# Kernel optimization log

Measured on AMD Instinct MI355X. Metric: run time of the kernel, lower is better.

The kernel has to match this reference:

```python
import jax, jax.numpy as jnp
import numpy as np
from jax import lax

N_HEADS = 16
EPS = 1e-6
CHUNK = 128  # chunk size for the causal kv cumsum scan


def causal_dot_product(q, k, v):
    """Equivalent to cumsum over outer-products: out[l] = q[l] . sum_{j<=l} k[j] v[j]^T.
    Chunked lax.scan avoids materializing the [B,H,L,D,M] tensor.
    q,k: [B,H,L,D], v: [B,H,L,M] -> [B,H,L,M]."""
    B, H, L, D = q.shape
    M = v.shape[-1]
    nc = L // CHUNK
    qc = q.reshape(B, H, nc, CHUNK, D).transpose(2, 0, 1, 3, 4)
    kc = k.reshape(B, H, nc, CHUNK, D).transpose(2, 0, 1, 3, 4)
    vc = v.reshape(B, H, nc, CHUNK, M).transpose(2, 0, 1, 3, 4)

    def step(kv_carry, inp):
        qb, kb, vb = inp  # [B,H,C,D], [B,H,C,D], [B,H,C,M]
        kv = jnp.einsum('bhcd,bhcm->bhcdm', kb, vb)
        kv_cum = jnp.cumsum(kv, axis=2) + kv_carry[:, :, None]
        out = jnp.einsum('bhcd,bhcdm->bhcm', qb, kv_cum)
        return kv_cum[:, :, -1], out

    init = jnp.zeros((B, H, D, M), q.dtype)
    _, outs = lax.scan(step, init, (qc, kc, vc))  # outs: [nc,B,H,C,M]
    return outs.transpose(1, 2, 0, 3, 4).reshape(B, H, L, M)


def flow_attention_causal(x, Wq, bq, Wk, bk, Wv, bv, Wo, bo):
    B, L, _ = x.shape
    d_model = Wq.shape[1]
    H = N_HEADS
    # projections -> [B,H,L,D]
    q = (x @ Wq + bq).reshape(B, L, H, -1).transpose(0, 2, 1, 3)
    k = (x @ Wk + bk).reshape(B, L, H, -1).transpose(0, 2, 1, 3)
    v = (x @ Wv + bv).reshape(B, L, H, -1).transpose(0, 2, 1, 3)
    # kernel_method = sigmoid
    q = jax.nn.sigmoid(q)
    k = jax.nn.sigmoid(k)

    sink_incoming = 1.0 / jnp.einsum('bhld,bhld->bhl', q + EPS, jnp.cumsum(k, axis=2) + EPS)
    source_outgoing = 1.0 / jnp.einsum('bhld,bhld->bhl', k + EPS, jnp.cumsum(q, axis=2) + EPS)
    normal = (jnp.arange(L, dtype=x.dtype) + 1.0)[None, None, :]  # [1,1,L]
    sink_incoming = sink_incoming * normal
    source_outgoing = source_outgoing * normal

    conserved_sink = jnp.einsum(
        'bhld,bhld->bhl', q + EPS,
        jnp.cumsum(k * source_outgoing[..., None], axis=2) + EPS) / normal
    conserved_source = jnp.einsum(
        'bhld,bhld->bhl', k + EPS,
        jnp.cumsum(q * sink_incoming[..., None], axis=2) + EPS) / normal

    sink_allocation = jax.nn.sigmoid(conserved_sink)
    cs = jnp.exp(conserved_source)
    source_competition = cs / jnp.cumsum(cs, axis=-1) * normal

    out = causal_dot_product(
        q * (sink_incoming / normal)[..., None],
        k,
        v * source_competition[..., None]) * sink_allocation[..., None]
    out = out.transpose(0, 2, 1, 3).reshape(B, L, d_model)
    return out @ Wo + bo  # dropout is identity at eval


def setup_inputs() -> dict:
    key = jax.random.key(0)
    ks = jax.random.split(key, 9)
    B, L, d_model = 4, 4096, 1024
    s = 0.02
    return {
        'x': jax.random.normal(ks[0], (B, L, d_model), dtype=jnp.float32),
        'Wq': jax.random.normal(ks[1], (d_model, d_model), dtype=jnp.float32) * s,
        'bq': jnp.zeros((d_model,), dtype=jnp.float32),
        'Wk': jax.random.normal(ks[2], (d_model, d_model), dtype=jnp.float32) * s,
        'bk': jnp.zeros((d_model,), dtype=jnp.float32),
        'Wv': jax.random.normal(ks[3], (d_model, d_model), dtype=jnp.float32) * s,
        'bv': jnp.zeros((d_model,), dtype=jnp.float32),
        'Wo': jax.random.normal(ks[4], (d_model, d_model), dtype=jnp.float32) * s,
        'bo': jnp.zeros((d_model,), dtype=jnp.float32),
    }


def reference(x, Wq, bq, Wk, bk, Wv, bv, Wo, bo):
    return flow_attention_causal(x, Wq, bq, Wk, bk, Wv, bv, Wo, bo)
```

## Files before the change

kernel.cpp:

```cpp
#include <hip/hip_runtime.h>
#include <stdint.h>

#define B_ 4
#define L_ 4096
#define DM 1024
#define H_ 16
#define D_ 64
#define BH (B_*H_)
#define N_ (B_*L_)
#define CS 128
#define NC (L_/CS)
#define SC 64
#define NSC (L_/SC)
#define EPSF 1e-6f

typedef unsigned short u16;
typedef unsigned int   u32;
typedef __attribute__((ext_vector_type(8))) short s16x8;
typedef __attribute__((ext_vector_type(4))) float f32x4;

__device__ __forceinline__ float bf2f(u16 u){
  union { u32 i; float f; } v; v.i = ((u32)u) << 16; return v.f;
}
__device__ __forceinline__ u16 f2bf(float f){
  union { float f; u32 i; } v; v.f = f;
  u32 i = v.i;
  return (u16)((i + 0x7fffu + ((i >> 16) & 1u)) >> 16);
}
__device__ __forceinline__ void gload16(const void* g, void* l){
  __builtin_amdgcn_global_load_lds(
      (const __attribute__((address_space(1))) u32*)g,
      (__attribute__((address_space(3))) u32*)l, 16, 0, 0);
}
__device__ __forceinline__ f32x4 mfma16(s16x8 a, s16x8 b, f32x4 c){
  return __builtin_amdgcn_mfma_f32_16x16x32_bf16(a, b, c, 0, 0, 0);
}
__device__ __forceinline__ float sigmoidf_(float x){ return 1.0f/(1.0f+__expf(-x)); }

__global__ void cvt_kernel(const float* __restrict__ in, u16* __restrict__ out, int n4){
  int i = blockIdx.x * blockDim.x + threadIdx.x;
  if (i >= n4) return;
  float4 v = ((const float4*)in)[i];
  union { u16 s[4]; uint2 u; } o;
  o.s[0]=f2bf(v.x); o.s[1]=f2bf(v.y); o.s[2]=f2bf(v.z); o.s[3]=f2bf(v.w);
  ((uint2*)out)[i] = o.u;
}

__global__ __launch_bounds__(256) void transpose_w4_kernel(
    const float* __restrict__ Wq, const float* __restrict__ Wk,
    const float* __restrict__ Wv, const float* __restrict__ Wo,
    u16* __restrict__ wqkvT, u16* __restrict__ woT){
  __shared__ float t[64][65];
  int z = blockIdx.z;
  const float* W = (z==0) ? Wq : (z==1) ? Wk : (z==2) ? Wv : Wo;
  u16* WT = (z<3) ? (wqkvT + (size_t)z*DM*DM) : woT;
  int n0 = blockIdx.x * 64, k0 = blockIdx.y * 64;
  int tx = threadIdx.x & 63, ty = threadIdx.x >> 6;
  #pragma unroll
  for (int s = 0; s < 64; s += 4)
    t[ty + s][tx] = W[(size_t)(k0 + ty + s) * DM + n0 + tx];
  __syncthreads();
  #pragma unroll
  for (int s = 0; s < 64; s += 4)
    WT[(size_t)(n0 + ty + s) * DM + k0 + tx] = f2bf(t[tx][ty + s]);
}

template<int QKV>
__global__ __launch_bounds__(512, 2) void gemm256_kernel(
    const u16* __restrict__ A, const u16* __restrict__ BT,
    const float* __restrict__ biasq, const float* __restrict__ biask, const float* __restrict__ biasv,
    u16* __restrict__ oq, u16* __restrict__ ok, u16* __restrict__ ov,
    float* __restrict__ outf,
    float* __restrict__ sumQ, float* __restrict__ sumK, int NBY)
{
  __shared__ __align__(16) u16 smem[65536];
  char* smb = (char*)smem;
  int tid = threadIdx.x;
  int wave = tid >> 6, lane = tid & 63;
  int wm = wave >> 2, wn = wave & 3;
  int nwg = gridDim.x;
  int q8 = nwg >> 3;
  int id = blockIdx.x;
  int id2 = (id & 7) * q8 + (id >> 3);
  int bx = id2 / NBY, by = id2 % NBY;
  int m0 = bx * 256, n0 = by * 256;
  int srcq = (tid & 7) ^ ((tid >> 3) & 7);
  const u16* aRow = A  + (size_t)(m0 + (tid >> 3)) * 1024 + srcq * 8;
  const u16* bRow = BT + (size_t)(n0 + (tid >> 3)) * 1024 + srcq * 8;

  f32x4 acc[8][4];
  #pragma unroll
  for (int i=0;i<8;i++)
    #pragma unroll
    for (int j=0;j<4;j++) acc[i][j] = (f32x4){0.f,0.f,0.f,0.f};

  int fr = lane & 15, q = lane >> 4;
  int aoff0 = fr*128 + (((q ^ (lane&3)) + 4*((lane>>2)&1)) << 4);
  int aoff1 = fr*128 + (((q ^ (lane&3)) + 4*(1 ^ ((lane>>2)&1))) << 4);

  #define STAGE(s, t) { \
    _Pragma("unroll") \
    for (int i_ = 0; i_ < 4; i_++){ \
      gload16(aRow + (size_t)(t)*64 + (size_t)i_*65536, smb + (s)*32768 + i_*8192 + tid*16); \
      gload16(bRow + (size_t)(t)*64 + (size_t)i_*65536, smb + 65536 + (s)*32768 + i_*8192 + tid*16); \
    } }

  #define COMPUTE(s) { \
    const char* Ab_ = smb + (s)*32768 + wm*16384; \
    const char* Bb_ = smb + 65536 + (s)*32768 + wn*8192; \
    _Pragma("unroll") \
    for (int kk_ = 0; kk_ < 2; kk_++){ \
      int off_ = kk_ ? aoff1 : aoff0; \
      s16x8 af_[8], bf_[4]; \
      _Pragma("unroll") \
      for (int mi_ = 0; mi_ < 8; mi_++) af_[mi_] = *(const s16x8*)(Ab_ + mi_*2048 + off_); \
      _Pragma("unroll") \
      for (int ni_ = 0; ni_ < 4; ni_++) bf_[ni_] = *(const s16x8*)(Bb_ + ni_*2048 + off_); \
      _Pragma("unroll") \
      for (int mi_ = 0; mi_ < 8; mi_++) \
        _Pragma("unroll") \
        for (int ni_ = 0; ni_ < 4; ni_++) \
          acc[mi_][ni_] = mfma16(af_[mi_], bf_[ni_], acc[mi_][ni_]); \
    } }

  STAGE(0, 0)
  STAGE(1, 1)
  for (int t = 0; t < 14; t++){
    asm volatile("s_waitcnt vmcnt(8)" ::: "memory");
    __builtin_amdgcn_s_barrier();
    asm volatile("" ::: "memory");
    COMPUTE(t & 1)
    asm volatile("s_waitcnt lgkmcnt(0)" ::: "memory");
    __builtin_amdgcn_s_barrier();
    asm volatile("" ::: "memory");
    STAGE(t & 1, t + 2)
  }
  asm volatile("s_waitcnt vmcnt(8)" ::: "memory");
  __builtin_amdgcn_s_barrier();
  asm volatile("" ::: "memory");
  COMPUTE(0)
  asm volatile("s_waitcnt vmcnt(0)" ::: "memory");
  __builtin_amdgcn_s_barrier();
  asm volatile("" ::: "memory");
  COMPUTE(1)

  int colblk = n0 + wn*64;
  int which  = QKV ? (colblk >> 10) : 0;
  int cl0    = QKV ? (colblk & 1023) : colblk;
  const float* bias = QKV ? (which==0 ? biasq : (which==1 ? biask : biasv)) : biasq;
  u16* outp = QKV ? (which==0 ? oq : (which==1 ? ok : ov)) : (u16*)0;
  float cs0[4] = {0.f,0.f,0.f,0.f}, cs1[4] = {0.f,0.f,0.f,0.f};
  #pragma unroll
  for (int mi = 0; mi < 8; mi++){
    int row = m0 + wm*128 + mi*16 + (lane>>4)*4;
    #pragma unroll
    for (int ni = 0; ni < 4; ni++){
      int cl = cl0 + ni*16 + fr;
      float bv = bias[cl];
      #pragma unroll
      for (int r = 0; r < 4; r++){
        float val = acc[mi][ni][r] + bv;
        if (QKV){
          if (which < 2) val = sigmoidf_(val);
          outp[(size_t)(row + r) * 1024 + cl] = f2bf(val);
          if (which < 2){ if (mi < 4) cs0[ni] += val; else cs1[ni] += val; }
        } else {
          outf[(size_t)(row + r) * 1024 + cl] = val;
        }
      }
    }
  }
  if (QKV && which < 2){
    float* sums = (which==0) ? sumQ : sumK;
    int bh = (m0 >> 12) * H_ + ((colblk & 1023) >> 6);
    int sc0 = ((m0 & 4095) >> 6) + wm*2;
    #pragma unroll
    for (int h2 = 0; h2 < 2; h2++){
      #pragma unroll
      for (int ni = 0; ni < 4; ni++){
        float s = h2 ? cs1[ni] : cs0[ni];
        s += __shfl_xor(s, 16);
        s += __shfl_xor(s, 32);
        if (lane < 16) sums[((size_t)bh*NSC + sc0 + h2)*64 + ni*16 + fr] = s;
      }
    }
  }
  #undef STAGE
  #undef COMPUTE
}

__global__ __launch_bounds__(64) void scan2_kernel(float* __restrict__ A, float* __restrict__ Bv){
  int bh = blockIdx.x, d = threadIdx.x;
  float ra = 0.f, rb = 0.f;
  for (int g = 0; g < NSC; g += 16){
    float ta[16], tb[16];
    #pragma unroll
    for (int j = 0; j < 16; j++){
      size_t o = ((size_t)bh * NSC + g + j) * 64 + d;
      ta[j] = A[o]; tb[j] = Bv[o];
    }
    #pragma unroll
    for (int j = 0; j < 16; j++){
      size_t o = ((size_t)bh * NSC + g + j) * 64 + d;
      A[o] = ra; Bv[o] = rb;
      ra += ta[j]; rb += tb[j];
    }
  }
}

__global__ __launch_bounds__(64) void siso_fused_kernel(
    const u16* __restrict__ q, const u16* __restrict__ k,
    const float* __restrict__ sumQx, const float* __restrict__ sumKx,
    float* __restrict__ si, float* __restrict__ so,
    float* __restrict__ sumQsi, float* __restrict__ sumKso)
{
  __shared__ u16 cq[64*64];
  __shared__ u16 ck[64*64];
  __shared__ float siv[64], sov[64];
  int bhc = blockIdx.x; int bh = bhc >> 6, sc = bhc & 63;
  int b = bh >> 4, h = bh & 15;
  int lane = threadIdx.x;
  size_t gbase = ((size_t)(b*L_ + sc*SC))*DM + h*D_;
  size_t lb = (size_t)bh*L_ + sc*SC;
  {
    float runQ = sumQx[bhc*64 + lane];
    float runK = sumKx[bhc*64 + lane];
    for (int l = 0; l < SC; l++){
      runQ += bf2f(q[gbase + (size_t)l*DM + lane]);
      runK += bf2f(k[gbase + (size_t)l*DM + lane]);
      int sw = lane ^ (l & 31);
      cq[l*64 + sw] = f2bf(runQ);
      ck[l*64 + sw] = f2bf(runK);
    }
  }
  __syncthreads();
  {
    int l = lane;
    const u16* qrow = q + gbase + (size_t)l*DM;
    const u16* krow = k + gbase + (size_t)l*DM;
    uint4 qr[8], kr[8];
    #pragma unroll
    for (int j=0;j<8;j++){ qr[j]=((const uint4*)qrow)[j]; kr[j]=((const uint4*)krow)[j]; }
    const u16* qp = (const u16*)qr; const u16* kp = (const u16*)kr;
    float a = 0.f, b2 = 0.f;
    #pragma unroll
    for (int d = 0; d < 64; d++){
      int sw = d ^ (l & 31);
      a  += (bf2f(qp[d])+EPSF) * (bf2f(ck[l*64+sw])+EPSF);
      b2 += (bf2f(kp[d])+EPSF) * (bf2f(cq[l*64+sw])+EPSF);
    }
    float n = (float)(sc*SC + l + 1);
    float vsi = n/a, vso = n/b2;
    si[lb+l] = vsi; so[lb+l] = vso;
    siv[l] = vsi;   sov[l] = vso;
  }
  __syncthreads();
  {
    float sq = 0.f, sk = 0.f;
    for (int l = 0; l < SC; l++){
      sq += bf2f(q[gbase + (size_t)l*DM + lane]) * siv[l];
      sk += bf2f(k[gbase + (size_t)l*DM + lane]) * sov[l];
    }
    sumQsi[bhc*64 + lane] = sq;
    sumKso[bhc*64 + lane] = sk;
  }
}

__global__ __launch_bounds__(64) void cons_fused_kernel(
    const u16* __restrict__ q, const u16* __restrict__ k,
    const float* __restrict__ si, const float* __restrict__ so,
    const float* __restrict__ sumQsiX, const float* __restrict__ sumKsoX,
    float* __restrict__ csrc, float* __restrict__ sall, float* __restrict__ csSum)
{
  __shared__ u16 cq[64*64];
  __shared__ u16 ck[64*64];
  __shared__ float siv[64], sov[64];
  int bhc = blockIdx.x; int bh = bhc >> 6, sc = bhc & 63;
  int b = bh >> 4, h = bh & 15;
  int lane = threadIdx.x;
  size_t gbase = ((size_t)(b*L_ + sc*SC))*DM + h*D_;
  size_t lb = (size_t)bh*L_ + sc*SC;
  siv[lane] = si[lb + lane];
  sov[lane] = so[lb + lane];
  __syncthreads();
  {
    float runQ = sumQsiX[bhc*64 + lane];
    float runK = sumKsoX[bhc*64 + lane];
    for (int l = 0; l < SC; l++){
      runQ += bf2f(q[gbase + (size_t)l*DM + lane]) * siv[l];
      runK += bf2f(k[gbase + (size_t)l*DM + lane]) * sov[l];
      int sw = lane ^ (l & 31);
      cq[l*64 + sw] = f2bf(runQ);
      ck[l*64 + sw] = f2bf(runK);
    }
  }
  __syncthreads();
  {
    int l = lane;
    const u16* qrow = q + gbase + (size_t)l*DM;
    const u16* krow = k + gbase + (size_t)l*DM;
    uint4 qr[8], kr[8];
    #pragma unroll
    for (int j=0;j<8;j++){ qr[j]=((const uint4*)qrow)[j]; kr[j]=((const uint4*)krow)[j]; }
    const u16* qp = (const u16*)qr; const u16* kp = (const u16*)kr;
    float a = 0.f, b2 = 0.f;
    #pragma unroll
    for (int d = 0; d < 64; d++){
      int sw = d ^ (l & 31);
      a  += (bf2f(qp[d])+EPSF) * (bf2f(ck[l*64+sw])+EPSF);
      b2 += (bf2f(kp[d])+EPSF) * (bf2f(cq[l*64+sw])+EPSF);
    }
    float inv = 1.0f / (float)(sc*SC + l + 1);
    sall[lb+l] = sigmoidf_(a * inv);
    float cs = b2 * inv;
    csrc[lb+l] = cs;
    float e = __expf(cs);
    #pragma unroll
    for (int off = 32; off > 0; off >>= 1) e += __shfl_xor(e, off);
    if (lane == 0) csSum[bhc] = e;
  }
}

__global__ __launch_bounds__(64) void cs_scan_kernel(const float* __restrict__ csSum, float* __restrict__ csOff){
  int bh = blockIdx.x; int lane = threadIdx.x;
  float v = csSum[bh * NSC + lane];
  float run = v;
  #pragma unroll
  for (int o = 1; o < 64; o <<= 1){
    float t = __shfl_up(run, o);
    if (lane >= o) run += t;
  }
  csOff[bh * NSC + lane] = run - v;
}

__global__ __launch_bounds__(64) void scomp_kernel(
    const float* __restrict__ csrc, const float* __restrict__ csOff,
    float* __restrict__ scomp){
  int bhc = blockIdx.x; int bh = bhc >> 6, sc = bhc & 63;
  int lane = threadIdx.x;
  size_t idx = (size_t)bh * L_ + sc * SC + lane;
  float cs = __expf(csrc[idx]);
  float run = cs;
  #pragma unroll
  for (int o = 1; o < 64; o <<= 1){
    float t = __shfl_up(run, o);
    if (lane >= o) run += t;
  }
  scomp[idx] = cs / (csOff[bh*NSC + sc] + run) * (float)(sc*SC + lane + 1);
}

__global__ __launch_bounds__(256) void vk_chunk_kernel(
    const u16* __restrict__ k, const u16* __restrict__ v,
    const float* __restrict__ scomp, float* __restrict__ vkc){
  __shared__ float ks[32][64];
  __shared__ float vs[32][64];
  int bhc = blockIdx.x; int bh = bhc >> 5, c = bhc & 31;
  int b = bh >> 4, h = bh & 15;
  int tid = threadIdx.x;
  int m = tid >> 2, d0 = (tid & 3) * 16;
  float acc[16];
  #pragma unroll
  for (int j = 0; j < 16; j++) acc[j] = 0.f;
  size_t gbase = ((size_t)(b * L_ + c * CS)) * DM + h * D_;
  size_t sbase = (size_t)bh * L_ + c * CS;
  int r = tid >> 3, cc = (tid & 7) * 8;
  for (int s0 = 0; s0 < CS; s0 += 32){
    __syncthreads();
    float sc = scomp[sbase + s0 + r];
    uint4 ku = *(const uint4*)(k + gbase + (size_t)(s0 + r) * DM + cc);
    uint4 vu = *(const uint4*)(v + gbase + (size_t)(s0 + r) * DM + cc);
    const u16* kp = (const u16*)&ku; const u16* vp = (const u16*)&vu;
    #pragma unroll
    for (int j = 0; j < 8; j++){
      ks[r][cc + j] = bf2f(kp[j]);
      vs[r][cc + j] = bf2f(vp[j]) * sc;
    }
    __syncthreads();
    #pragma unroll
    for (int i = 0; i < 32; i++){
      float vm = vs[i][m];
      #pragma unroll
      for (int j4 = 0; j4 < 4; j4++){
        float4 kk = *(const float4*)&ks[i][d0 + j4*4];
        acc[j4*4+0] += vm * kk.x; acc[j4*4+1] += vm * kk.y;
        acc[j4*4+2] += vm * kk.z; acc[j4*4+3] += vm * kk.w;
      }
    }
  }
  float* outp = vkc + (size_t)bhc * (D_*D_) + m * D_ + d0;
  #pragma unroll
  for (int j = 0; j < 16; j++) outp[j] = acc[j];
}

__global__ __launch_bounds__(256) void vk_scan_kernel(float* __restrict__ vkc){
  int idx = blockIdx.x * 256 + threadIdx.x;
  int bh = idx >> 12;
  int e  = idx & 4095;
  size_t base = ((size_t)bh * NC) * 4096 + e;
  float run = 0.f;
  for (int g = 0; g < NC; g += 16){
    float tv[16];
    #pragma unroll
    for (int j = 0; j < 16; j++) tv[j] = vkc[base + (size_t)(g + j) * 4096];
    #pragma unroll
    for (int j = 0; j < 16; j++){
      vkc[base + (size_t)(g + j) * 4096] = run;
      run += tv[j];
    }
  }
}

__global__ __launch_bounds__(256) void attn_kernel(
    const u16* __restrict__ q, const u16* __restrict__ k, const u16* __restrict__ v,
    const float* __restrict__ si, const float* __restrict__ scomp, const float* __restrict__ salloc,
    const float* __restrict__ vkc, u16* __restrict__ attnout)
{
  __shared__ __align__(16) u16 qs[128*64];
  __shared__ __align__(16) u16 ks2[128*64];
  __shared__ __align__(16) u16 vts[64*128];
  __shared__ __align__(16) u16 vks[64*64];
  __shared__ __align__(16) u16 ss[128*32];
  int bhc = blockIdx.x; int bh = bhc >> 5, c = bhc & 31;
  int b = bh >> 4, h = bh & 15;
  int tid = threadIdx.x, wave = tid >> 6, lane = tid & 63;
  size_t gbase = ((size_t)(b * L_ + c * CS)) * DM + h * D_;
  size_t sbase = (size_t)bh * L_ + c * CS;
  {
    int r = tid >> 1;
    int cc = (tid & 1) * 32;
    int l = c * CS + r;
    float qscale = si[sbase + r] / (float)(l + 1);
    float vscale = scomp[sbase + r];
    #pragma unroll
    for (int j = 0; j < 4; j++){
      uint4 qu = *(const uint4*)(q + gbase + (size_t)r * DM + cc + j*8);
      uint4 kuv = *(const uint4*)(k + gbase + (size_t)r * DM + cc + j*8);
      uint4 vu = *(const uint4*)(v + gbase + (size_t)r * DM + cc + j*8);
      const u16* qp = (const u16*)&qu; const u16* vp = (const u16*)&vu;
      u16 tmp[8];
      #pragma unroll
      for (int e = 0; e < 8; e++) tmp[e] = f2bf(bf2f(qp[e]) * qscale);
      *(uint4*)&qs[r*64 + cc + j*8] = *(uint4*)tmp;
      *(uint4*)&ks2[r*64 + cc + j*8] = kuv;
      #pragma unroll
      for (int e = 0; e < 8; e++) vts[(cc + j*8 + e)*128 + r] = f2bf(bf2f(vp[e]) * vscale);
    }
    const float* vkp = vkc + (size_t)bhc * (D_*D_) + tid * 16;
    u16 tv[16];
    #pragma unroll
    for (int e = 0; e < 16; e++) tv[e] = f2bf(vkp[e]);
    *(uint4*)&vks[tid*16]   = *(uint4*)&tv[0];
    *(uint4*)&vks[tid*16+8] = *(uint4*)&tv[8];
  }
  __syncthreads();
  int t0 = wave, t1 = 7 - wave;
  int fr = lane & 15, kg = (lane >> 4) * 8;
  f32x4 acc[2][4];
  #pragma unroll
  for (int i=0;i<2;i++)
    #pragma unroll
    for (int j=0;j<4;j++) acc[i][j] = (f32x4){0.f,0.f,0.f,0.f};
  s16x8 aq[2][2];
  #pragma unroll
  for (int ti = 0; ti < 2; ti++){
    int t = ti ? t1 : t0;
    #pragma unroll
    for (int kk = 0; kk < 2; kk++)
      aq[ti][kk] = *(const s16x8*)&qs[(t*16 + fr)*64 + kk*32 + kg];
  }
  #pragma unroll
  for (int mt = 0; mt < 4; mt++){
    #pragma unroll
    for (int kk = 0; kk < 2; kk++){
      s16x8 bv = *(const s16x8*)&vks[(mt*16 + fr)*64 + kk*32 + kg];
      acc[0][mt] = mfma16(aq[0][kk], bv, acc[0][mt]);
      acc[1][mt] = mfma16(aq[1][kk], bv, acc[1][mt]);
    }
  }
  for (int jt = 0; jt < 4; jt++){
    __syncthreads();
    #pragma unroll
    for (int ti = 0; ti < 2; ti++){
      int t = ti ? t1 : t0;
      #pragma unroll
      for (int u = 0; u < 2; u++){
        int jj = jt*2 + u;
        f32x4 sacc = (f32x4){0.f,0.f,0.f,0.f};
        if (jj <= t){
          #pragma unroll
          for (int kk = 0; kk < 2; kk++){
            s16x8 bkf = *(const s16x8*)&ks2[(jj*16 + fr)*64 + kk*32 + kg];
            sacc = mfma16(aq[ti][kk], bkf, sacc);
          }
        }
        int lrow = t*16 + (lane>>4)*4;
        int jcol = jj*16 + fr;
        #pragma unroll
        for (int r = 0; r < 4; r++){
          float sv = (jcol <= lrow + r) ? sacc[r] : 0.f;
          ss[(lrow + r)*32 + u*16 + fr] = f2bf(sv);
        }
      }
    }
    __syncthreads();
    #pragma unroll
    for (int ti = 0; ti < 2; ti++){
      int t = ti ? t1 : t0;
      if (jt*32 <= t*16 + 15){
        s16x8 as = *(const s16x8*)&ss[(t*16 + fr)*32 + kg];
        #pragma unroll
        for (int mt = 0; mt < 4; mt++){
          s16x8 bvv = *(const s16x8*)&vts[(mt*16 + fr)*128 + jt*32 + kg];
          acc[ti][mt] = mfma16(as, bvv, acc[ti][mt]);
        }
      }
    }
  }
  #pragma unroll
  for (int ti = 0; ti < 2; ti++){
    int t = ti ? t1 : t0;
    int lrow = t*16 + (lane>>4)*4;
    #pragma unroll
    for (int r = 0; r < 4; r++){
      float sa = salloc[sbase + lrow + r];
      size_t orow = ((size_t)(b * L_ + c * CS + lrow + r)) * DM + h * D_;
      #pragma unroll
      for (int mt = 0; mt < 4; mt++){
        attnout[orow + mt*16 + fr] = f2bf(acc[ti][mt][r] * sa);
      }
    }
  }
}

extern "C" void kernel_launch(void* const* d_in, const int* in_sizes, int n_in,
                              void* d_out, int out_size, void* d_ws, size_t ws_size,
                              hipStream_t stream){
  (void)in_sizes; (void)n_in; (void)out_size; (void)ws_size;
  const float* x  = (const float*)d_in[0];
  const float* Wq = (const float*)d_in[1];
  const float* bq = (const float*)d_in[2];
  const float* Wk = (const float*)d_in[3];
  const float* bk = (const float*)d_in[4];
  const float* Wv = (const float*)d_in[5];
  const float* bv = (const float*)d_in[6];
  const float* Wo = (const float*)d_in[7];
  const float* bo = (const float*)d_in[8];

  char* p = (char*)d_ws;
  auto carve = [&](size_t bytes) -> void* {
    void* r = (void*)p; p += (bytes + 255) & ~(size_t)255; return r;
  };
  u16* xb    = (u16*)carve((size_t)N_*DM*2);
  u16* wqkvT = (u16*)carve((size_t)3*DM*DM*2);
  u16* woT   = (u16*)carve((size_t)DM*DM*2);
  u16* qb  = (u16*)carve((size_t)N_*DM*2);
  u16* kb  = (u16*)carve((size_t)N_*DM*2);
  u16* vb  = (u16*)carve((size_t)N_*DM*2);
  u16* ao  = (u16*)carve((size_t)N_*DM*2);
  float* si   = (float*)carve((size_t)BH*L_*4);
  float* so   = (float*)carve((size_t)BH*L_*4);
  float* csrc = (float*)carve((size_t)BH*L_*4);
  float* sall = (float*)carve((size_t)BH*L_*4);
  float* scmp = (float*)carve((size_t)BH*L_*4);
  float* sumQ   = (float*)carve((size_t)BH*NSC*D_*4);
  float* sumK   = (float*)carve((size_t)BH*NSC*D_*4);
  float* sumQsi = (float*)carve((size_t)BH*NSC*D_*4);
  float* sumKso = (float*)carve((size_t)BH*NSC*D_*4);
  float* csSum  = (float*)carve((size_t)BH*NSC*4);
  float* csOff  = (float*)carve((size_t)BH*NSC*4);
  float* vkc    = (float*)carve((size_t)BH*NC*(size_t)(D_*D_)*4);

  cvt_kernel<<<(N_*DM/4 + 255)/256, 256, 0, stream>>>(x, xb, N_*DM/4);
  transpose_w4_kernel<<<dim3(DM/64, DM/64, 4), 256, 0, stream>>>(Wq, Wk, Wv, Wo, wqkvT, woT);
  gemm256_kernel<1><<<dim3((N_/256)*(3*DM/256)), 512, 0, stream>>>(
      xb, wqkvT, bq, bk, bv, qb, kb, vb, nullptr, sumQ, sumK, 3*DM/256);
  scan2_kernel<<<BH, 64, 0, stream>>>(sumQ, sumK);
  siso_fused_kernel<<<BH*NSC, 64, 0, stream>>>(qb, kb, sumQ, sumK, si, so, sumQsi, sumKso);
  scan2_kernel<<<BH, 64, 0, stream>>>(sumQsi, sumKso);
  cons_fused_kernel<<<BH*NSC, 64, 0, stream>>>(qb, kb, si, so, sumQsi, sumKso, csrc, sall, csSum);
  cs_scan_kernel<<<BH, 64, 0, stream>>>(csSum, csOff);
  scomp_kernel<<<BH*NSC, 64, 0, stream>>>(csrc, csOff, scmp);
  vk_chunk_kernel<<<BH*NC, 256, 0, stream>>>(kb, vb, scmp, vkc);
  vk_scan_kernel<<<(BH*D_*D_)/256, 256, 0, stream>>>(vkc);
  attn_kernel<<<BH*NC, 256, 0, stream>>>(qb, kb, vb, si, scmp, sall, vkc, ao);
  gemm256_kernel<0><<<dim3((N_/256)*(DM/256)), 512, 0, stream>>>(
      ao, woT, bo, bo, bo, nullptr, nullptr, nullptr, (float*)d_out, nullptr, nullptr, DM/256);
}
```

Baseline: 368.2 us.

## Reuse LDS tiles in siso, fold cs scan into scomp, widen attn score tiles

In siso_fused_kernel the q/k rows already held in registers are written into the swizzled shared tiles, so the column sums read LDS instead of re-reading global memory. The separate cs_scan kernel is removed and each scomp block computes its own prefix offset with a masked wave reduction, saving one launch and a buffer. attn_kernel now builds 64-column score tiles in two outer iterations instead of 32-column tiles in four, halving the __syncthreads count at the cost of a larger ss shared buffer. The new __syncthreads inside the per-lane block in siso is a risk if only some threads reach it.

```diff
diff --git a/kernel.cpp b/kernel.cpp
--- a/kernel.cpp
+++ b/kernel.cpp
@@ -253,13 +253,21 @@
     float vsi = n/a, vso = n/b2;
     si[lb+l] = vsi; so[lb+l] = vso;
     siv[l] = vsi;   sov[l] = vso;
+    __syncthreads();
+    #pragma unroll
+    for (int d = 0; d < 64; d++){
+      int sw = d ^ (l & 31);
+      cq[l*64 + sw] = qp[d];
+      ck[l*64 + sw] = kp[d];
+    }
   }
   __syncthreads();
   {
     float sq = 0.f, sk = 0.f;
     for (int l = 0; l < SC; l++){
-      sq += bf2f(q[gbase + (size_t)l*DM + lane]) * siv[l];
-      sk += bf2f(k[gbase + (size_t)l*DM + lane]) * sov[l];
+      int sw = lane ^ (l & 31);
+      sq += bf2f(cq[l*64 + sw]) * siv[l];
+      sk += bf2f(ck[l*64 + sw]) * sov[l];
     }
     sumQsi[bhc*64 + lane] = sq;
     sumKso[bhc*64 + lane] = sk;
@@ -321,32 +329,24 @@
   }
 }
 
-__global__ __launch_bounds__(64) void cs_scan_kernel(const float* __restrict__ csSum, float* __restrict__ csOff){
-  int bh = blockIdx.x; int lane = threadIdx.x;
-  float v = csSum[bh * NSC + lane];
-  float run = v;
+__global__ __launch_bounds__(64) void scomp_kernel(
+    const float* __restrict__ csrc, const float* __restrict__ csSum,
+    float* __restrict__ scomp){
+  int bhc = blockIdx.x; int bh = bhc >> 6, sc = bhc & 63;
+  int lane = threadIdx.x;
+  float v2 = (lane < sc) ? csSum[bh*NSC + lane] : 0.f;
+  #pragma unroll
+  for (int o = 32; o > 0; o >>= 1) v2 += __shfl_xor(v2, o);
+  float off = v2;
+  size_t idx = (size_t)bh * L_ + sc * SC + lane;
+  float cs = __expf(csrc[idx]);
+  float run = cs;
   #pragma unroll
   for (int o = 1; o < 64; o <<= 1){
     float t = __shfl_up(run, o);
     if (lane >= o) run += t;
   }
-  csOff[bh * NSC + lane] = run - v;
-}
-
-__global__ __launch_bounds__(64) void scomp_kernel(
-    const float* __restrict__ csrc, const float* __restrict__ csOff,
-    float* __restrict__ scomp){
-  int bhc = blockIdx.x; int bh = bhc >> 6, sc = bhc & 63;
-  int lane = threadIdx.x;
-  size_t idx = (size_t)bh * L_ + sc * SC + lane;
-  float cs = __expf(csrc[idx]);
-  float run = cs;
-  #pragma unroll
-  for (int o = 1; o < 64; o <<= 1){
-    float t = __shfl_up(run, o);
-    if (lane >= o) run += t;
-  }
-  scomp[idx] = cs / (csOff[bh*NSC + sc] + run) * (float)(sc*SC + lane + 1);
+  scomp[idx] = cs / (off + run) * (float)(sc*SC + lane + 1);
 }
 
 __global__ __launch_bounds__(256) void vk_chunk_kernel(
@@ -419,7 +419,7 @@
   __shared__ __align__(16) u16 ks2[128*64];
   __shared__ __align__(16) u16 vts[64*128];
   __shared__ __align__(16) u16 vks[64*64];
-  __shared__ __align__(16) u16 ss[128*32];
+  __shared__ __align__(16) u16 ss[128*64];
   int bhc = blockIdx.x; int bh = bhc >> 5, c = bhc & 31;
   int b = bh >> 4, h = bh & 15;
   int tid = threadIdx.x, wave = tid >> 6, lane = tid & 63;
@@ -477,14 +477,14 @@
       acc[1][mt] = mfma16(aq[1][kk], bv, acc[1][mt]);
     }
   }
-  for (int jt = 0; jt < 4; jt++){
+  for (int jt2 = 0; jt2 < 2; jt2++){
     __syncthreads();
     #pragma unroll
     for (int ti = 0; ti < 2; ti++){
       int t = ti ? t1 : t0;
       #pragma unroll
-      for (int u = 0; u < 2; u++){
-        int jj = jt*2 + u;
+      for (int u = 0; u < 4; u++){
+        int jj = jt2*4 + u;
         f32x4 sacc = (f32x4){0.f,0.f,0.f,0.f};
         if (jj <= t){
           #pragma unroll
@@ -498,7 +498,7 @@
         #pragma unroll
         for (int r = 0; r < 4; r++){
           float sv = (jcol <= lrow + r) ? sacc[r] : 0.f;
-          ss[(lrow + r)*32 + u*16 + fr] = f2bf(sv);
+          ss[(lrow + r)*64 + u*16 + fr] = f2bf(sv);
         }
       }
     }
@@ -506,12 +506,15 @@
     #pragma unroll
     for (int ti = 0; ti < 2; ti++){
       int t = ti ? t1 : t0;
-      if (jt*32 <= t*16 + 15){
-        s16x8 as = *(const s16x8*)&ss[(t*16 + fr)*32 + kg];
-        #pragma unroll
-        for (int mt = 0; mt < 4; mt++){
-          s16x8 bvv = *(const s16x8*)&vts[(mt*16 + fr)*128 + jt*32 + kg];
-          acc[ti][mt] = mfma16(as, bvv, acc[ti][mt]);
+      #pragma unroll
+      for (int ks = 0; ks < 2; ks++){
+        if (jt2*64 + ks*32 <= t*16 + 15){
+          s16x8 as = *(const s16x8*)&ss[(t*16 + fr)*64 + ks*32 + kg];
+          #pragma unroll
+          for (int mt = 0; mt < 4; mt++){
+            s16x8 bvv = *(const s16x8*)&vts[(mt*16 + fr)*128 + jt2*64 + ks*32 + kg];
+            acc[ti][mt] = mfma16(as, bvv, acc[ti][mt]);
+          }
         }
       }
     }
@@ -567,7 +570,6 @@
   float* sumQsi = (float*)carve((size_t)BH*NSC*D_*4);
   float* sumKso = (float*)carve((size_t)BH*NSC*D_*4);
   float* csSum  = (float*)carve((size_t)BH*NSC*4);
-  float* csOff  = (float*)carve((size_t)BH*NSC*4);
   float* vkc    = (float*)carve((size_t)BH*NC*(size_t)(D_*D_)*4);
 
   cvt_kernel<<<(N_*DM/4 + 255)/256, 256, 0, stream>>>(x, xb, N_*DM/4);
@@ -578,8 +580,7 @@
   siso_fused_kernel<<<BH*NSC, 64, 0, stream>>>(qb, kb, sumQ, sumK, si, so, sumQsi, sumKso);
   scan2_kernel<<<BH, 64, 0, stream>>>(sumQsi, sumKso);
   cons_fused_kernel<<<BH*NSC, 64, 0, stream>>>(qb, kb, si, so, sumQsi, sumKso, csrc, sall, csSum);
-  cs_scan_kernel<<<BH, 64, 0, stream>>>(csSum, csOff);
-  scomp_kernel<<<BH*NSC, 64, 0, stream>>>(csrc, csOff, scmp);
+  scomp_kernel<<<BH*NSC, 64, 0, stream>>>(csrc, csSum, scmp);
   vk_chunk_kernel<<<BH*NC, 256, 0, stream>>>(kb, vb, scmp, vkc);
   vk_scan_kernel<<<(BH*D_*D_)/256, 256, 0, stream>>>(vkc);
   attn_kernel<<<BH*NC, 256, 0, stream>>>(qb, kb, vb, si, scmp, sall, vkc, ao);
```

Measured after the change: 364.6 us. No clear change (-1.0%).
